# Kernel tuning notes

Hardware: AMD Instinct MI355X
Metric: run time of the kernel (lower is better)

The kernel has to match this reference:

```python
import jax, jax.numpy as jnp
import numpy as np

BN_EPS = 1e-5


def setup_inputs() -> dict:
    key = jax.random.key(0)
    ks = jax.random.split(key, 8)
    N, Cin, Cout, D, H, W = 4, 512, 256, 256, 128, 128
    feat_ffm = jax.random.normal(ks[0], (N, Cin, H, W), dtype=jnp.float32)
    coarse_x = jax.random.normal(ks[1], (N, D, H, W), dtype=jnp.float32)
    # conv1: 1x1, no bias; BN (eval mode: running stats); conv2: 1x1 with bias
    w1 = jax.random.normal(ks[2], (Cout, Cin), dtype=jnp.float32) * (1.0 / np.sqrt(Cin))
    bn_gamma = jnp.ones((Cout,), dtype=jnp.float32)
    bn_beta = jnp.zeros((Cout,), dtype=jnp.float32)
    bn_mean = jax.random.normal(ks[3], (Cout,), dtype=jnp.float32) * 0.1
    bn_var = jax.random.uniform(ks[4], (Cout,), dtype=jnp.float32, minval=0.5, maxval=1.5)
    w2 = jax.random.normal(ks[5], (Cout, Cout), dtype=jnp.float32) * (1.0 / np.sqrt(Cout))
    b2 = jnp.zeros((Cout,), dtype=jnp.float32)
    return {"feat_ffm": feat_ffm, "coarse_x": coarse_x, "w1": w1,
            "bn_gamma": bn_gamma, "bn_beta": bn_beta, "bn_mean": bn_mean,
            "bn_var": bn_var, "w2": w2, "b2": b2}


def reference(feat_ffm, coarse_x, w1, bn_gamma, bn_beta, bn_mean, bn_var, w2, b2):
    N, D, H, W = coarse_x.shape
    # conv1 (1x1) + BN(eval) + ReLU; Dropout2d is identity in eval mode
    x = jnp.einsum('nihw,oi->nohw', feat_ffm, w1)
    scale = bn_gamma * jax.lax.rsqrt(bn_var + BN_EPS)
    x = x * scale[None, :, None, None] + (bn_beta - bn_mean * scale)[None, :, None, None]
    x = jax.nn.relu(x)  # [N, C, H, W]
    C = x.shape[1]
    q = coarse_x.reshape(N, D, H * W)          # proj_query / proj_value
    k = x.reshape(N, C, H * W)                 # proj_key (pre-permute)
    energy = jnp.einsum('nds,ncs->ndc', q, k)  # [N, D, C]
    energy_new = jnp.max(energy, axis=-1, keepdims=True) - energy
    attention = jax.nn.softmax(energy_new, axis=-1)        # [N, D, C]
    out = jnp.einsum('ndc,nds->ncs', attention, q)         # attention^T @ value
    out = out.reshape(N, C, H, W)
    out = jnp.einsum('nchw,oc->nohw', out, w2) + b2[None, :, None, None]
    return out
```

## Files before the change

### kernel.cpp

```cpp
#include <hip/hip_runtime.h>


#define S_DIM 16384
#define C_DIM 256
#define CIN 512

typedef unsigned short u16;
typedef __attribute__((ext_vector_type(8))) short bf16x8;
typedef __attribute__((ext_vector_type(4))) float f32x4;

__device__ __forceinline__ u16 f2bf(float x) {
    unsigned u = __float_as_uint(x);
    u += 0x7fff + ((u >> 16) & 1);
    return (u16)(u >> 16);
}
__device__ __forceinline__ float bf2f(u16 h) {
    return __uint_as_float(((unsigned)h) << 16);
}
__device__ __forceinline__ void gld16(const u16* g, u16* l) {
    __builtin_amdgcn_global_load_lds((const __attribute__((address_space(1))) void*)g,
                                     (__attribute__((address_space(3))) void*)l, 16, 0, 0);
}
__device__ __forceinline__ void gld4(const float* g, float* l) {
    __builtin_amdgcn_global_load_lds((const __attribute__((address_space(1))) void*)g,
                                     (__attribute__((address_space(3))) void*)l, 4, 0, 0);
}

__global__ __launch_bounds__(256) void prep_kernel(
    const float* __restrict__ coarse, const float* __restrict__ w1,
    const float* __restrict__ gamma, const float* __restrict__ beta,
    const float* __restrict__ mean, const float* __restrict__ var,
    u16* __restrict__ qhi, u16* __restrict__ qlo,
    u16* __restrict__ w1hi, u16* __restrict__ w1lo, float* __restrict__ b1) {
    int b = blockIdx.x;
    int t = threadIdx.x;
    if (b < 4096) {
        size_t i = (size_t)b * 256 + t;
        for (size_t c = i; c < 4194304u; c += 1048576u) {
            float4 v = ((const float4*)coarse)[c];
            float vv[4] = {v.x, v.y, v.z, v.w};
            u16 h[4], l[4];
#pragma unroll
            for (int j = 0; j < 4; ++j) {
                h[j] = f2bf(vv[j]);
                l[j] = f2bf(vv[j] - bf2f(h[j]));
            }
            *(uint2*)&qhi[c * 4] = *(uint2*)h;
            *(uint2*)&qlo[c * 4] = *(uint2*)l;
        }
    } else {
        int o = (b - 4096) * 16 + (t >> 4);
        int lane16 = t & 15;
        float sc = gamma[o] * rsqrtf(var[o] + 1e-5f);
        for (int i = lane16; i < CIN; i += 16) {
            float v = w1[o * CIN + i] * sc;
            u16 h = f2bf(v);
            w1hi[o * CIN + i] = h;
            w1lo[o * CIN + i] = f2bf(v - bf2f(h));
        }
        if (lane16 == 0) b1[o] = beta[o] - mean[o] * sc;
    }
}

__global__ __launch_bounds__(256) void conv_kernel(
    const u16* __restrict__ w1hi, const u16* __restrict__ w1lo,
    const float* __restrict__ feat, const float* __restrict__ b1,
    u16* __restrict__ khi, u16* __restrict__ klo) {
    __shared__ u16 AhS[4096], AlS[4096];
    __shared__ float BfS[32 * 133];
    int s0 = blockIdx.x * 128;
    int m0 = blockIdx.y * 128;
    int bz = blockIdx.z;
    int tid = threadIdx.x, wave = tid >> 6, lane = tid & 63;

    int c0 = wave * 128 + lane, c1 = c0 + 64;
    int r0 = c0 >> 2, k0 = (c0 & 3) * 8;
    int r1 = c1 >> 2, k1 = (c1 & 3) * 8;
    const u16* gA0h = w1hi + (size_t)(m0 + r0) * CIN + k0;
    const u16* gA1h = w1hi + (size_t)(m0 + r1) * CIN + k1;
    const u16* gA0l = w1lo + (size_t)(m0 + r0) * CIN + k0;
    const u16* gA1l = w1lo + (size_t)(m0 + r1) * CIN + k1;
    const float* fB = feat + (size_t)bz * ((size_t)CIN * S_DIM) + s0 + lane;

    int quad = lane >> 4, l15 = lane & 15;
    int wm = wave >> 1, wn = wave & 1;
    int aBase = (wm * 64 + l15) * 32 + quad * 8;

    f32x4 zero = {0.f, 0.f, 0.f, 0.f};
    f32x4 acc[4][4];
#pragma unroll
    for (int i = 0; i < 4; ++i)
#pragma unroll
        for (int j = 0; j < 4; ++j) acc[i][j] = zero;

    for (int kb = 0; kb < CIN; kb += 32) {
        __syncthreads();
        gld16(gA0h, AhS + c0 * 8);
        gld16(gA1h, AhS + c1 * 8);
        gld16(gA0l, AlS + c0 * 8);
        gld16(gA1l, AlS + c1 * 8);
        gA0h += 32; gA1h += 32; gA0l += 32; gA1l += 32;
#pragma unroll
        for (int j = 0; j < 16; ++j) {
            int cc = wave * 16 + j;
            int i = cc >> 1, h = cc & 1;
            gld4(fB + (size_t)(kb + i) * S_DIM + h * 64, BfS + i * 133 + h * 64 + lane);
        }
        __syncthreads();

        bf16x8 a_h[4], a_l[4];
#pragma unroll
        for (int t = 0; t < 4; ++t) {
            a_h[t] = *(const bf16x8*)&AhS[aBase + t * 512];
            a_l[t] = *(const bf16x8*)&AlS[aBase + t * 512];
        }
        bf16x8 b_h[4], b_l[4];
#pragma unroll
        for (int nt = 0; nt < 4; ++nt) {
            int n = wn * 64 + nt * 16 + l15;
            union { u16 u[8]; bf16x8 v; } th, tl;
#pragma unroll
            for (int j = 0; j < 8; ++j) {
                float f = BfS[(quad * 8 + j) * 133 + n];
                u16 h = f2bf(f);
                th.u[j] = h;
                tl.u[j] = (u16)(__float_as_uint(f - bf2f(h)) >> 16);
            }
            b_h[nt] = th.v;
            b_l[nt] = tl.v;
        }
#pragma unroll
        for (int mt = 0; mt < 4; ++mt)
#pragma unroll
            for (int nt = 0; nt < 4; ++nt) {
                acc[mt][nt] = __builtin_amdgcn_mfma_f32_16x16x32_bf16(a_h[mt], b_h[nt], acc[mt][nt], 0, 0, 0);
                acc[mt][nt] = __builtin_amdgcn_mfma_f32_16x16x32_bf16(a_h[mt], b_l[nt], acc[mt][nt], 0, 0, 0);
                acc[mt][nt] = __builtin_amdgcn_mfma_f32_16x16x32_bf16(a_l[mt], b_h[nt], acc[mt][nt], 0, 0, 0);
            }
    }

#pragma unroll
    for (int mt = 0; mt < 4; ++mt) {
#pragma unroll
        for (int r = 0; r < 4; ++r) {
            int row = m0 + wm * 64 + mt * 16 + quad * 4 + r;
            float bi = b1[row];
#pragma unroll
            for (int nt = 0; nt < 4; ++nt) {
                int cc = s0 + wn * 64 + nt * 16 + l15;
                float v = fmaxf(acc[mt][nt][r] + bi, 0.f);
                u16 h = f2bf(v);
                size_t o = (size_t)bz * 4194304 + (size_t)row * S_DIM + cc;
                khi[o] = h;
                klo[o] = f2bf(v - bf2f(h));
            }
        }
    }
}

__global__ __launch_bounds__(256) void energy_kernel(
    const u16* __restrict__ qhi, const u16* __restrict__ qlo,
    const u16* __restrict__ khi, const u16* __restrict__ klo,
    float* __restrict__ Ep) {
    __shared__ u16 AhS[4096], BhS[4096], AlS[4096], BlS[4096];
    int kBeg = blockIdx.x * 256;
    int m0 = (blockIdx.y >> 1) * 128;
    int n0 = (blockIdx.y & 1) * 128;
    int bz = blockIdx.z;
    int tid = threadIdx.x, wave = tid >> 6, lane = tid & 63;

    int c0 = wave * 128 + lane, c1 = c0 + 64;
    int r0 = c0 >> 2, k0 = (c0 & 3) * 8;
    int r1 = c1 >> 2, k1 = (c1 & 3) * 8;
    size_t bo = (size_t)bz * 4194304;
    const u16* gA0h = qhi + bo + (size_t)(m0 + r0) * S_DIM + kBeg + k0;
    const u16* gA1h = qhi + bo + (size_t)(m0 + r1) * S_DIM + kBeg + k1;
    const u16* gB0h = khi + bo + (size_t)(n0 + r0) * S_DIM + kBeg + k0;
    const u16* gB1h = khi + bo + (size_t)(n0 + r1) * S_DIM + kBeg + k1;
    const u16* gA0l = qlo + bo + (size_t)(m0 + r0) * S_DIM + kBeg + k0;
    const u16* gA1l = qlo + bo + (size_t)(m0 + r1) * S_DIM + kBeg + k1;
    const u16* gB0l = klo + bo + (size_t)(n0 + r0) * S_DIM + kBeg + k0;
    const u16* gB1l = klo + bo + (size_t)(n0 + r1) * S_DIM + kBeg + k1;

    int quad = lane >> 4, l15 = lane & 15;
    int wm = wave >> 1, wn = wave & 1;
    int aBase = (wm * 64 + l15) * 32 + quad * 8;
    int bBase = (wn * 64 + l15) * 32 + quad * 8;

    f32x4 zero = {0.f, 0.f, 0.f, 0.f};
    f32x4 acc[4][4];
#pragma unroll
    for (int i = 0; i < 4; ++i)
#pragma unroll
        for (int j = 0; j < 4; ++j) acc[i][j] = zero;

    for (int kb = 0; kb < 256; kb += 32) {
        __syncthreads();
        gld16(gA0h, AhS + c0 * 8);
        gld16(gA1h, AhS + c1 * 8);
        gld16(gB0h, BhS + c0 * 8);
        gld16(gB1h, BhS + c1 * 8);
        gld16(gA0l, AlS + c0 * 8);
        gld16(gA1l, AlS + c1 * 8);
        gld16(gB0l, BlS + c0 * 8);
        gld16(gB1l, BlS + c1 * 8);
        gA0h += 32; gA1h += 32; gB0h += 32; gB1h += 32;
        gA0l += 32; gA1l += 32; gB0l += 32; gB1l += 32;
        __syncthreads();

        bf16x8 a_h[4], b_h[4], a_l[4], b_l[4];
#pragma unroll
        for (int t = 0; t < 4; ++t) {
            a_h[t] = *(const bf16x8*)&AhS[aBase + t * 512];
            b_h[t] = *(const bf16x8*)&BhS[bBase + t * 512];
            a_l[t] = *(const bf16x8*)&AlS[aBase + t * 512];
            b_l[t] = *(const bf16x8*)&BlS[bBase + t * 512];
        }
#pragma unroll
        for (int mt = 0; mt < 4; ++mt)
#pragma unroll
            for (int nt = 0; nt < 4; ++nt) {
                acc[mt][nt] = __builtin_amdgcn_mfma_f32_16x16x32_bf16(a_h[mt], b_h[nt], acc[mt][nt], 0, 0, 0);
                acc[mt][nt] = __builtin_amdgcn_mfma_f32_16x16x32_bf16(a_h[mt], b_l[nt], acc[mt][nt], 0, 0, 0);
                acc[mt][nt] = __builtin_amdgcn_mfma_f32_16x16x32_bf16(a_l[mt], b_h[nt], acc[mt][nt], 0, 0, 0);
            }
    }

    float* Ce = Ep + ((size_t)(blockIdx.x * 4 + bz)) * 65536;
#pragma unroll
    for (int mt = 0; mt < 4; ++mt)
#pragma unroll
        for (int r = 0; r < 4; ++r) {
            int row = m0 + wm * 64 + mt * 16 + quad * 4 + r;
#pragma unroll
            for (int nt = 0; nt < 4; ++nt) {
                int cc = n0 + wn * 64 + nt * 16 + l15;
                Ce[(size_t)row * C_DIM + cc] = acc[mt][nt][r];
            }
        }
}

__global__ __launch_bounds__(256) void softmax_kernel(const float* __restrict__ Ep,
                                                      float* __restrict__ att) {
    __shared__ float red[4], red2[4];
    int b = blockIdx.x;
    int t = threadIdx.x;
    const float* p = Ep + (size_t)b * 256 + t;
    float v = 0.f;
#pragma unroll 8
    for (int s = 0; s < 64; ++s) v += p[(size_t)s * 262144];
    float m = v;
#pragma unroll
    for (int o = 32; o > 0; o >>= 1) m = fminf(m, __shfl_xor(m, o, 64));
    int lane = t & 63, wid = t >> 6;
    if (lane == 0) red[wid] = m;
    __syncthreads();
    m = fminf(fminf(red[0], red[1]), fminf(red[2], red[3]));
    float e = expf(m - v);
    float s = e;
#pragma unroll
    for (int o = 32; o > 0; o >>= 1) s += __shfl_xor(s, o, 64);
    if (lane == 0) red2[wid] = s;
    __syncthreads();
    s = red2[0] + red2[1] + red2[2] + red2[3];
    att[(size_t)b * 256 + t] = e / s;
}

__global__ __launch_bounds__(256) void m2h_kernel(const float* __restrict__ w2,
                                                  const float* __restrict__ att,
                                                  u16* __restrict__ M2h) {
    int t = blockIdx.x * 256 + threadIdx.x;
    int d = t & 255, o = (t >> 8) & 255, n = t >> 16;
    const float4* wr = (const float4*)(w2 + (size_t)o * C_DIM);
    const float4* ar = (const float4*)(att + ((size_t)n * C_DIM + d) * C_DIM);
    float s = 0.0f;
#pragma unroll 4
    for (int c4 = 0; c4 < 64; ++c4) {
        float4 w = wr[c4];
        float4 a = ar[c4];
        s += w.x * a.x + w.y * a.y + w.z * a.z + w.w * a.w;
    }
    M2h[((size_t)n * C_DIM + o) * C_DIM + d] = f2bf(s);
}

__global__ __launch_bounds__(256) void final_kernel(
    const u16* __restrict__ M2h, const float* __restrict__ coarse,
    const float* __restrict__ b2, float* __restrict__ out) {
    __shared__ u16 AhS[4096];
    __shared__ float BfS[32 * 133];
    int s0 = blockIdx.x * 128;
    int m0 = blockIdx.y * 128;
    int bz = blockIdx.z;
    int tid = threadIdx.x, wave = tid >> 6, lane = tid & 63;

    int c0 = wave * 128 + lane, c1 = c0 + 64;
    int r0 = c0 >> 2, k0 = (c0 & 3) * 8;
    int r1 = c1 >> 2, k1 = (c1 & 3) * 8;
    const u16* gA0 = M2h + (size_t)bz * 65536 + (size_t)(m0 + r0) * C_DIM + k0;
    const u16* gA1 = M2h + (size_t)bz * 65536 + (size_t)(m0 + r1) * C_DIM + k1;
    const float* fB = coarse + (size_t)bz * 4194304 + s0 + lane;

    int quad = lane >> 4, l15 = lane & 15;
    int wm = wave >> 1, wn = wave & 1;
    int aBase = (wm * 64 + l15) * 32 + quad * 8;

    f32x4 zero = {0.f, 0.f, 0.f, 0.f};
    f32x4 acc[4][4];
#pragma unroll
    for (int i = 0; i < 4; ++i)
#pragma unroll
        for (int j = 0; j < 4; ++j) acc[i][j] = zero;

    for (int kb = 0; kb < C_DIM; kb += 32) {
        __syncthreads();
        gld16(gA0, AhS + c0 * 8);
        gld16(gA1, AhS + c1 * 8);
        gA0 += 32; gA1 += 32;
#pragma unroll
        for (int j = 0; j < 16; ++j) {
            int cc = wave * 16 + j;
            int i = cc >> 1, h = cc & 1;
            gld4(fB + (size_t)(kb + i) * S_DIM + h * 64, BfS + i * 133 + h * 64 + lane);
        }
        __syncthreads();

        bf16x8 a_h[4];
#pragma unroll
        for (int t = 0; t < 4; ++t) a_h[t] = *(const bf16x8*)&AhS[aBase + t * 512];
        bf16x8 b_h[4];
#pragma unroll
        for (int nt = 0; nt < 4; ++nt) {
            int n = wn * 64 + nt * 16 + l15;
            union { u16 u[8]; bf16x8 v; } th;
#pragma unroll
            for (int j = 0; j < 8; ++j) th.u[j] = f2bf(BfS[(quad * 8 + j) * 133 + n]);
            b_h[nt] = th.v;
        }
#pragma unroll
        for (int mt = 0; mt < 4; ++mt)
#pragma unroll
            for (int nt = 0; nt < 4; ++nt)
                acc[mt][nt] = __builtin_amdgcn_mfma_f32_16x16x32_bf16(a_h[mt], b_h[nt], acc[mt][nt], 0, 0, 0);
    }

#pragma unroll
    for (int mt = 0; mt < 4; ++mt)
#pragma unroll
        for (int r = 0; r < 4; ++r) {
            int row = m0 + wm * 64 + mt * 16 + quad * 4 + r;
            float bi = b2[row];
#pragma unroll
            for (int nt = 0; nt < 4; ++nt) {
                int cc = s0 + wn * 64 + nt * 16 + l15;
                out[(size_t)bz * 4194304 + (size_t)row * S_DIM + cc] = acc[mt][nt][r] + bi;
            }
        }
}

extern "C" void kernel_launch(void* const* d_in, const int* in_sizes, int n_in,
                              void* d_out, int out_size, void* d_ws, size_t ws_size,
                              hipStream_t stream) {
    const float* feat   = (const float*)d_in[0];
    const float* coarse = (const float*)d_in[1];
    const float* w1     = (const float*)d_in[2];
    const float* gamma  = (const float*)d_in[3];
    const float* beta   = (const float*)d_in[4];
    const float* mean   = (const float*)d_in[5];
    const float* var    = (const float*)d_in[6];
    const float* w2     = (const float*)d_in[7];
    const float* b2     = (const float*)d_in[8];
    float* out = (float*)d_out;

    char* base = (char*)d_ws;
    u16* qhi   = (u16*)(base);
    u16* qlo   = (u16*)(base + 33554432);
    u16* khi   = (u16*)(base + 67108864);
    u16* klo   = (u16*)(base + 100663296);
    float* Ep  = (float*)(base + 134217728);
    float* att = (float*)(base + 201326592);
    u16* M2h   = (u16*)(base + 202375168);
    u16* w1hi  = (u16*)(base + 202899456);
    u16* w1lo  = (u16*)(base + 203161600);
    float* b1  = (float*)(base + 203423744);

    prep_kernel<<<4112, 256, 0, stream>>>(coarse, w1, gamma, beta, mean, var,
                                          qhi, qlo, w1hi, w1lo, b1);

    conv_kernel<<<dim3(128, 2, 4), 256, 0, stream>>>(w1hi, w1lo, feat, b1, khi, klo);

    energy_kernel<<<dim3(64, 4, 4), 256, 0, stream>>>(qhi, qlo, khi, klo, Ep);

    softmax_kernel<<<1024, 256, 0, stream>>>(Ep, att);

    m2h_kernel<<<1024, 256, 0, stream>>>(w2, att, M2h);

    final_kernel<<<dim3(128, 2, 4), 256, 0, stream>>>(M2h, coarse, b2, out);
}
```

Baseline: 447.0 us.

## Use 16-byte LDS staging with k-major swizzled layout and halve energy split-K

Global-to-LDS loads of the fp32 B operands in the conv and final GEMMs now move 16 bytes per lane instead of 4, into a k-major LDS layout with an XOR swizzle that avoids bank conflicts. The A-tile staging is reorganised so each wave loads one 8-wide k slice for 64 rows. The bf16 split conversion is done two values at a time with byte_perm packing. The energy kernel's split-K chunk doubles to 512, which halves the partial-sum workspace traffic and the number of blocks, with a matching change to the softmax reduction count. The cost is fewer blocks in the energy launch.

```diff
diff --git a/kernel.cpp b/kernel.cpp
--- a/kernel.cpp
+++ b/kernel.cpp
@@ -21,9 +21,9 @@
     __builtin_amdgcn_global_load_lds((const __attribute__((address_space(1))) void*)g,
                                      (__attribute__((address_space(3))) void*)l, 16, 0, 0);
 }
-__device__ __forceinline__ void gld4(const float* g, float* l) {
+__device__ __forceinline__ void gld16f(const float* g, float* l) {
     __builtin_amdgcn_global_load_lds((const __attribute__((address_space(1))) void*)g,
-                                     (__attribute__((address_space(3))) void*)l, 4, 0, 0);
+                                     (__attribute__((address_space(3))) void*)l, 16, 0, 0);
 }
 
 __global__ __launch_bounds__(256) void prep_kernel(
@@ -67,24 +67,24 @@
     const float* __restrict__ feat, const float* __restrict__ b1,
     u16* __restrict__ khi, u16* __restrict__ klo) {
     __shared__ u16 AhS[4096], AlS[4096];
-    __shared__ float BfS[32 * 133];
+    __shared__ float BfS[4096];
     int s0 = blockIdx.x * 128;
     int m0 = blockIdx.y * 128;
     int bz = blockIdx.z;
     int tid = threadIdx.x, wave = tid >> 6, lane = tid & 63;
-
-    int c0 = wave * 128 + lane, c1 = c0 + 64;
-    int r0 = c0 >> 2, k0 = (c0 & 3) * 8;
-    int r1 = c1 >> 2, k1 = (c1 & 3) * 8;
-    const u16* gA0h = w1hi + (size_t)(m0 + r0) * CIN + k0;
-    const u16* gA1h = w1hi + (size_t)(m0 + r1) * CIN + k1;
-    const u16* gA0l = w1lo + (size_t)(m0 + r0) * CIN + k0;
-    const u16* gA1l = w1lo + (size_t)(m0 + r1) * CIN + k1;
-    const float* fB = feat + (size_t)bz * ((size_t)CIN * S_DIM) + s0 + lane;
-
     int quad = lane >> 4, l15 = lane & 15;
     int wm = wave >> 1, wn = wave & 1;
-    int aBase = (wm * 64 + l15) * 32 + quad * 8;
+
+    const u16* gAh0 = w1hi + (size_t)(m0 + lane) * CIN + wave * 8;
+    const u16* gAh1 = w1hi + (size_t)(m0 + 64 + lane) * CIN + wave * 8;
+    const u16* gAl0 = w1lo + (size_t)(m0 + lane) * CIN + wave * 8;
+    const u16* gAl1 = w1lo + (size_t)(m0 + 64 + lane) * CIN + wave * 8;
+    u16* dAh = AhS + wave * 1024;
+    u16* dAl = AlS + wave * 1024;
+    int bcol = ((lane & 31) * 4) ^ ((wave & 1) << 4);
+    const float* gB = feat + (size_t)bz * ((size_t)CIN * S_DIM)
+                    + (size_t)(8 * wave + (lane >> 5)) * S_DIM + s0 + bcol;
+    float* dB = BfS + wave * 1024;
 
     f32x4 zero = {0.f, 0.f, 0.f, 0.f};
     f32x4 acc[4][4];
@@ -95,39 +95,45 @@
 
     for (int kb = 0; kb < CIN; kb += 32) {
         __syncthreads();
-        gld16(gA0h, AhS + c0 * 8);
-        gld16(gA1h, AhS + c1 * 8);
-        gld16(gA0l, AlS + c0 * 8);
-        gld16(gA1l, AlS + c1 * 8);
-        gA0h += 32; gA1h += 32; gA0l += 32; gA1l += 32;
-#pragma unroll
-        for (int j = 0; j < 16; ++j) {
-            int cc = wave * 16 + j;
-            int i = cc >> 1, h = cc & 1;
-            gld4(fB + (size_t)(kb + i) * S_DIM + h * 64, BfS + i * 133 + h * 64 + lane);
-        }
+        gld16(gAh0 + kb, dAh);
+        gld16(gAh1 + kb, dAh + 512);
+        gld16(gAl0 + kb, dAl);
+        gld16(gAl1 + kb, dAl + 512);
+#pragma unroll
+        for (int p = 0; p < 4; ++p)
+            gld16f(gB + (size_t)(kb + 2 * p) * S_DIM, dB + p * 256);
         __syncthreads();
 
         bf16x8 a_h[4], a_l[4];
+        int aOff = quad * 1024 + (wm * 64 + l15) * 8;
 #pragma unroll
         for (int t = 0; t < 4; ++t) {
-            a_h[t] = *(const bf16x8*)&AhS[aBase + t * 512];
-            a_l[t] = *(const bf16x8*)&AlS[aBase + t * 512];
+            a_h[t] = *(const bf16x8*)&AhS[aOff + t * 128];
+            a_l[t] = *(const bf16x8*)&AlS[aOff + t * 128];
         }
         bf16x8 b_h[4], b_l[4];
+        int fl = (quad & 1) << 4;
+        const float* Brow = BfS + quad * 1024;
 #pragma unroll
         for (int nt = 0; nt < 4; ++nt) {
-            int n = wn * 64 + nt * 16 + l15;
-            union { u16 u[8]; bf16x8 v; } th, tl;
-#pragma unroll
-            for (int j = 0; j < 8; ++j) {
-                float f = BfS[(quad * 8 + j) * 133 + n];
-                u16 h = f2bf(f);
-                th.u[j] = h;
-                tl.u[j] = (u16)(__float_as_uint(f - bf2f(h)) >> 16);
-            }
-            b_h[nt] = th.v;
-            b_l[nt] = tl.v;
+            int nf = (wn * 64 + nt * 16 + l15) ^ fl;
+            union { unsigned d[4]; bf16x8 v; } H, L;
+#pragma unroll
+            for (int d = 0; d < 4; ++d) {
+                float fa = Brow[(2 * d) * 128 + nf];
+                float fb = Brow[(2 * d + 1) * 128 + nf];
+                unsigned ua = __float_as_uint(fa), ub = __float_as_uint(fb);
+                unsigned ra = ua + 0x7fffu + ((ua >> 16) & 1);
+                unsigned rb = ub + 0x7fffu + ((ub >> 16) & 1);
+                H.d[d] = __byte_perm(ra, rb, 0x7632);
+                unsigned la = __float_as_uint(fa - __uint_as_float(ra & 0xffff0000u));
+                unsigned lb = __float_as_uint(fb - __uint_as_float(rb & 0xffff0000u));
+                la += 0x7fffu + ((la >> 16) & 1);
+                lb += 0x7fffu + ((lb >> 16) & 1);
+                L.d[d] = __byte_perm(la, lb, 0x7632);
+            }
+            b_h[nt] = H.v;
+            b_l[nt] = L.v;
         }
 #pragma unroll
         for (int mt = 0; mt < 4; ++mt)
@@ -163,29 +169,27 @@
     const u16* __restrict__ khi, const u16* __restrict__ klo,
     float* __restrict__ Ep) {
     __shared__ u16 AhS[4096], BhS[4096], AlS[4096], BlS[4096];
-    int kBeg = blockIdx.x * 256;
+    int kBeg = blockIdx.x * 512;
     int m0 = (blockIdx.y >> 1) * 128;
     int n0 = (blockIdx.y & 1) * 128;
     int bz = blockIdx.z;
     int tid = threadIdx.x, wave = tid >> 6, lane = tid & 63;
-
-    int c0 = wave * 128 + lane, c1 = c0 + 64;
-    int r0 = c0 >> 2, k0 = (c0 & 3) * 8;
-    int r1 = c1 >> 2, k1 = (c1 & 3) * 8;
-    size_t bo = (size_t)bz * 4194304;
-    const u16* gA0h = qhi + bo + (size_t)(m0 + r0) * S_DIM + kBeg + k0;
-    const u16* gA1h = qhi + bo + (size_t)(m0 + r1) * S_DIM + kBeg + k1;
-    const u16* gB0h = khi + bo + (size_t)(n0 + r0) * S_DIM + kBeg + k0;
-    const u16* gB1h = khi + bo + (size_t)(n0 + r1) * S_DIM + kBeg + k1;
-    const u16* gA0l = qlo + bo + (size_t)(m0 + r0) * S_DIM + kBeg + k0;
-    const u16* gA1l = qlo + bo + (size_t)(m0 + r1) * S_DIM + kBeg + k1;
-    const u16* gB0l = klo + bo + (size_t)(n0 + r0) * S_DIM + kBeg + k0;
-    const u16* gB1l = klo + bo + (size_t)(n0 + r1) * S_DIM + kBeg + k1;
-
     int quad = lane >> 4, l15 = lane & 15;
     int wm = wave >> 1, wn = wave & 1;
-    int aBase = (wm * 64 + l15) * 32 + quad * 8;
-    int bBase = (wn * 64 + l15) * 32 + quad * 8;
+
+    size_t bo = (size_t)bz * 4194304;
+    const u16* gAh0 = qhi + bo + (size_t)(m0 + lane) * S_DIM + kBeg + wave * 8;
+    const u16* gAh1 = qhi + bo + (size_t)(m0 + 64 + lane) * S_DIM + kBeg + wave * 8;
+    const u16* gAl0 = qlo + bo + (size_t)(m0 + lane) * S_DIM + kBeg + wave * 8;
+    const u16* gAl1 = qlo + bo + (size_t)(m0 + 64 + lane) * S_DIM + kBeg + wave * 8;
+    const u16* gBh0 = khi + bo + (size_t)(n0 + lane) * S_DIM + kBeg + wave * 8;
+    const u16* gBh1 = khi + bo + (size_t)(n0 + 64 + lane) * S_DIM + kBeg + wave * 8;
+    const u16* gBl0 = klo + bo + (size_t)(n0 + lane) * S_DIM + kBeg + wave * 8;
+    const u16* gBl1 = klo + bo + (size_t)(n0 + 64 + lane) * S_DIM + kBeg + wave * 8;
+    u16* dAh = AhS + wave * 1024;
+    u16* dAl = AlS + wave * 1024;
+    u16* dBh = BhS + wave * 1024;
+    u16* dBl = BlS + wave * 1024;
 
     f32x4 zero = {0.f, 0.f, 0.f, 0.f};
     f32x4 acc[4][4];
@@ -194,27 +198,27 @@
 #pragma unroll
         for (int j = 0; j < 4; ++j) acc[i][j] = zero;
 
-    for (int kb = 0; kb < 256; kb += 32) {
-        __syncthreads();
-        gld16(gA0h, AhS + c0 * 8);
-        gld16(gA1h, AhS + c1 * 8);
-        gld16(gB0h, BhS + c0 * 8);
-        gld16(gB1h, BhS + c1 * 8);
-        gld16(gA0l, AlS + c0 * 8);
-        gld16(gA1l, AlS + c1 * 8);
-        gld16(gB0l, BlS + c0 * 8);
-        gld16(gB1l, BlS + c1 * 8);
-        gA0h += 32; gA1h += 32; gB0h += 32; gB1h += 32;
-        gA0l += 32; gA1l += 32; gB0l += 32; gB1l += 32;
+    for (int kb = 0; kb < 512; kb += 32) {
+        __syncthreads();
+        gld16(gAh0 + kb, dAh);
+        gld16(gAh1 + kb, dAh + 512);
+        gld16(gBh0 + kb, dBh);
+        gld16(gBh1 + kb, dBh + 512);
+        gld16(gAl0 + kb, dAl);
+        gld16(gAl1 + kb, dAl + 512);
+        gld16(gBl0 + kb, dBl);
+        gld16(gBl1 + kb, dBl + 512);
         __syncthreads();
 
         bf16x8 a_h[4], b_h[4], a_l[4], b_l[4];
+        int aOff = quad * 1024 + (wm * 64 + l15) * 8;
+        int bOff = quad * 1024 + (wn * 64 + l15) * 8;
 #pragma unroll
         for (int t = 0; t < 4; ++t) {
-            a_h[t] = *(const bf16x8*)&AhS[aBase + t * 512];
-            b_h[t] = *(const bf16x8*)&BhS[bBase + t * 512];
-            a_l[t] = *(const bf16x8*)&AlS[aBase + t * 512];
-            b_l[t] = *(const bf16x8*)&BlS[bBase + t * 512];
+            a_h[t] = *(const bf16x8*)&AhS[aOff + t * 128];
+            b_h[t] = *(const bf16x8*)&BhS[bOff + t * 128];
+            a_l[t] = *(const bf16x8*)&AlS[aOff + t * 128];
+            b_l[t] = *(const bf16x8*)&BlS[bOff + t * 128];
         }
 #pragma unroll
         for (int mt = 0; mt < 4; ++mt)
@@ -248,7 +252,7 @@
     const float* p = Ep + (size_t)b * 256 + t;
     float v = 0.f;
 #pragma unroll 8
-    for (int s = 0; s < 64; ++s) v += p[(size_t)s * 262144];
+    for (int s = 0; s < 32; ++s) v += p[(size_t)s * 262144];
     float m = v;
 #pragma unroll
     for (int o = 32; o > 0; o >>= 1) m = fminf(m, __shfl_xor(m, o, 64));
@@ -287,22 +291,21 @@
     const u16* __restrict__ M2h, const float* __restrict__ coarse,
     const float* __restrict__ b2, float* __restrict__ out) {
     __shared__ u16 AhS[4096];
-    __shared__ float BfS[32 * 133];
+    __shared__ float BfS[4096];
     int s0 = blockIdx.x * 128;
     int m0 = blockIdx.y * 128;
     int bz = blockIdx.z;
     int tid = threadIdx.x, wave = tid >> 6, lane = tid & 63;
-
-    int c0 = wave * 128 + lane, c1 = c0 + 64;
-    int r0 = c0 >> 2, k0 = (c0 & 3) * 8;
-    int r1 = c1 >> 2, k1 = (c1 & 3) * 8;
-    const u16* gA0 = M2h + (size_t)bz * 65536 + (size_t)(m0 + r0) * C_DIM + k0;
-    const u16* gA1 = M2h + (size_t)bz * 65536 + (size_t)(m0 + r1) * C_DIM + k1;
-    const float* fB = coarse + (size_t)bz * 4194304 + s0 + lane;
-
     int quad = lane >> 4, l15 = lane & 15;
     int wm = wave >> 1, wn = wave & 1;
-    int aBase = (wm * 64 + l15) * 32 + quad * 8;
+
+    const u16* gA0 = M2h + (size_t)bz * 65536 + (size_t)(m0 + lane) * C_DIM + wave * 8;
+    const u16* gA1 = M2h + (size_t)bz * 65536 + (size_t)(m0 + 64 + lane) * C_DIM + wave * 8;
+    u16* dA = AhS + wave * 1024;
+    int bcol = ((lane & 31) * 4) ^ ((wave & 1) << 4);
+    const float* gB = coarse + (size_t)bz * 4194304
+                    + (size_t)(8 * wave + (lane >> 5)) * S_DIM + s0 + bcol;
+    float* dB = BfS + wave * 1024;
 
     f32x4 zero = {0.f, 0.f, 0.f, 0.f};
     f32x4 acc[4][4];
@@ -313,28 +316,34 @@
 
     for (int kb = 0; kb < C_DIM; kb += 32) {
         __syncthreads();
-        gld16(gA0, AhS + c0 * 8);
-        gld16(gA1, AhS + c1 * 8);
-        gA0 += 32; gA1 += 32;
-#pragma unroll
-        for (int j = 0; j < 16; ++j) {
-            int cc = wave * 16 + j;
-            int i = cc >> 1, h = cc & 1;
-            gld4(fB + (size_t)(kb + i) * S_DIM + h * 64, BfS + i * 133 + h * 64 + lane);
-        }
+        gld16(gA0 + kb, dA);
+        gld16(gA1 + kb, dA + 512);
+#pragma unroll
+        for (int p = 0; p < 4; ++p)
+            gld16f(gB + (size_t)(kb + 2 * p) * S_DIM, dB + p * 256);
         __syncthreads();
 
         bf16x8 a_h[4];
-#pragma unroll
-        for (int t = 0; t < 4; ++t) a_h[t] = *(const bf16x8*)&AhS[aBase + t * 512];
+        int aOff = quad * 1024 + (wm * 64 + l15) * 8;
+#pragma unroll
+        for (int t = 0; t < 4; ++t) a_h[t] = *(const bf16x8*)&AhS[aOff + t * 128];
         bf16x8 b_h[4];
+        int fl = (quad & 1) << 4;
+        const float* Brow = BfS + quad * 1024;
 #pragma unroll
         for (int nt = 0; nt < 4; ++nt) {
-            int n = wn * 64 + nt * 16 + l15;
-            union { u16 u[8]; bf16x8 v; } th;
-#pragma unroll
-            for (int j = 0; j < 8; ++j) th.u[j] = f2bf(BfS[(quad * 8 + j) * 133 + n]);
-            b_h[nt] = th.v;
+            int nf = (wn * 64 + nt * 16 + l15) ^ fl;
+            union { unsigned d[4]; bf16x8 v; } H;
+#pragma unroll
+            for (int d = 0; d < 4; ++d) {
+                float fa = Brow[(2 * d) * 128 + nf];
+                float fb = Brow[(2 * d + 1) * 128 + nf];
+                unsigned ua = __float_as_uint(fa), ub = __float_as_uint(fb);
+                unsigned ra = ua + 0x7fffu + ((ua >> 16) & 1);
+                unsigned rb = ub + 0x7fffu + ((ub >> 16) & 1);
+                H.d[d] = __byte_perm(ra, rb, 0x7632);
+            }
+            b_h[nt] = H.v;
         }
 #pragma unroll
         for (int mt = 0; mt < 4; ++mt)
@@ -388,7 +397,7 @@
 
     conv_kernel<<<dim3(128, 2, 4), 256, 0, stream>>>(w1hi, w1lo, feat, b1, khi, klo);
 
-    energy_kernel<<<dim3(64, 4, 4), 256, 0, stream>>>(qhi, qlo, khi, klo, Ep);
+    energy_kernel<<<dim3(32, 4, 4), 256, 0, stream>>>(qhi, qlo, khi, klo, Ep);
 
     softmax_kernel<<<1024, 256, 0, stream>>>(Ep, att);
 
```

Result: slower. 460.4 us (+3.0%).
